# Kernel tuning notes

Measured on AMD Instinct MI355X. Metric: run time of the kernel, lower is better.

## Reference

```python
import jax, jax.numpy as jnp
import numpy as np

KERNEL = 3  # kernel_size from init_kwargs


def _unfold(x, k):
    """torch.nn.functional.unfold with padding=k//2, stride=1.
    Returns [b, c*k*k, h*w] with torch's ordering: index = c*(k*k) + kh*k + kw.
    """
    b, c, h, w = x.shape
    p = k // 2
    xp = jnp.pad(x, ((0, 0), (0, 0), (p, p), (p, p)))
    # fixed k*k = 9 slices (small static loop, not a data-dim loop)
    cols = jnp.stack(
        [xp[:, :, i:i + h, j:j + w] for i in range(k) for j in range(k)],
        axis=2,
    )  # [b, c, k*k, h, w]
    return cols.reshape(b, c * k * k, h * w)


def setup_inputs() -> dict:
    key = jax.random.key(0)
    k1, k2 = jax.random.split(key)
    x = jax.random.normal(k1, (8, 64, 128, 128), dtype=jnp.float32)
    # memory parameter: torch.rand -> uniform [0, 1), shape [c*k*k, out_channels]
    memory = jax.random.uniform(k2, (64 * KERNEL * KERNEL, 128), dtype=jnp.float32)
    return {"x": x, "memory": memory}


def reference(x, memory):
    b, c, h, w = x.shape
    cols = _unfold(x, KERNEL)                 # [b, c*k*k, h*w]
    cols = jax.nn.softmax(cols, axis=1)       # softmax over unfolded patch dim
    out = jnp.einsum('ki,bkl->bil', memory, cols)  # [b, out_ch, h*w]
    return out.reshape(b, memory.shape[1], h, w)
```

## Files before the change

kernel.cpp:

```cpp
#include <hip/hip_runtime.h>
#include <stdint.h>


#define Bn 8
#define Cn 64
#define Hn 128
#define Wn 128
#define OC 128
#define HW (Hn * Wn)

typedef __attribute__((ext_vector_type(8))) short bf16x8_t;
typedef __attribute__((ext_vector_type(4))) float f32x4_t;

__device__ inline unsigned short f2bf(float f) {
    union { float f; uint32_t u; } v; v.f = f;
    uint32_t u = v.u;
    u += 0x7fffu + ((u >> 16) & 1u);
    return (unsigned short)(u >> 16);
}
__device__ inline float bf2f(unsigned short h) {
    union { uint32_t u; float f; } v; v.u = ((uint32_t)h) << 16;
    return v.f;
}

__global__ void prep_b(const float* __restrict__ mem, unsigned short* __restrict__ Bt) {
    int kin = blockIdx.x;
    int n = threadIdx.x;
    int c = kin / 9, q = kin % 9;
    Bt[n * 576 + q * 64 + c] = f2bf(mem[kin * OC + n]);
}

__global__ __launch_bounds__(256) void exp_tr(const float* __restrict__ x,
                                              unsigned short* __restrict__ Et,
                                              float* __restrict__ S) {
    __shared__ __align__(16) unsigned short lds[128][72];
    int bid = blockIdx.x;
    int b = bid >> 7, h = bid & 127;
    int t = threadIdx.x;

    int c = t >> 2, l4 = t & 3;
    const float* xp = x + ((size_t)(b * Cn + c) * Hn + h) * Wn;
#pragma unroll
    for (int i = 0; i < 8; i++) {
        int w = i * 16 + l4 * 4;
        float4 v = *(const float4*)(xp + w);
        lds[w + 0][c] = f2bf(__expf(v.x));
        lds[w + 1][c] = f2bf(__expf(v.y));
        lds[w + 2][c] = f2bf(__expf(v.z));
        lds[w + 3][c] = f2bf(__expf(v.w));
    }
    __syncthreads();

    {
        int w = t >> 1, c0 = (t & 1) * 32;
        uint4* dst = (uint4*)(Et + (((size_t)(b * Hn + h) * Wn + w) * 64 + c0));
        const uint4* src = (const uint4*)(&lds[w][c0]);
        dst[0] = src[0]; dst[1] = src[1]; dst[2] = src[2]; dst[3] = src[3];
    }
    if (t < 128) {
        int w = t;
        float s = 0.f;
#pragma unroll
        for (int c2 = 0; c2 < 64; c2++) s += bf2f(lds[w][c2]);
        S[(size_t)(b * Hn + h) * Wn + w] = s;
    }
}

__global__ void boxz(const float* __restrict__ S, float* __restrict__ Zinv) {
    int p = blockIdx.x * 256 + threadIdx.x;
    int b = p >> 14, r = p & 16383, h = r >> 7, w = r & 127;
    const float* Sp = S + (size_t)b * HW;
    float z = 0.f;
#pragma unroll
    for (int dh = -1; dh <= 1; dh++) {
        int hh = h + dh;
#pragma unroll
        for (int dw = -1; dw <= 1; dw++) {
            int ww = w + dw;
            if (hh >= 0 && hh < Hn && ww >= 0 && ww < Wn)
                z += Sp[hh * Wn + ww];
            else
                z += 64.0f;
        }
    }
    Zinv[p] = 1.f / z;
}

__global__ __launch_bounds__(256) void conv_mfma(const unsigned short* __restrict__ Et,
                                                 const unsigned short* __restrict__ Bt,
                                                 const float* __restrict__ Zinv,
                                                 float* __restrict__ out) {
    __shared__ __align__(16) unsigned short lds[6 * 18 * 72];

    int bid = blockIdx.x;
    int b = bid >> 8;
    int rem = bid & 255;
    int ty = rem >> 3;
    int tx = rem & 7;
    int h0 = ty * 4, w0 = tx * 16;
    int t = threadIdx.x;

    {
        int pp = t >> 3;
        int c0 = (t & 7) * 8;
        const uint4 ones = make_uint4(0x3F803F80u, 0x3F803F80u, 0x3F803F80u, 0x3F803F80u);
#pragma unroll
        for (int rr = 0; rr < 4; rr++) {
            int p = pp + rr * 32;
            if (p < 108) {
                int y = p / 18, xx = p % 18;
                int gh = h0 - 1 + y, gw = w0 - 1 + xx;
                uint4 v = ones;
                if (gh >= 0 && gh < Hn && gw >= 0 && gw < Wn)
                    v = *(const uint4*)(Et + (((size_t)(b * Hn + gh) * Wn + gw) * 64 + c0));
                *(uint4*)(&lds[(y * 18 + xx) * 72 + c0]) = v;
            }
        }
    }
    __syncthreads();

    int wave = t >> 6, lane = t & 63;
    int mcol = lane & 15;
    int quad = lane >> 4;
    int koff = quad * 8;

    f32x4_t acc[4][2];
#pragma unroll
    for (int i = 0; i < 4; i++)
#pragma unroll
        for (int j = 0; j < 2; j++) acc[i][j] = (f32x4_t){0.f, 0.f, 0.f, 0.f};

    int n_base = wave * 32;

    for (int kc = 0; kc < 18; kc++) {
        int q = kc >> 1;
        int c0 = (kc & 1) * 32;
        int kh = q / 3, kw = q % 3;

        bf16x8_t a[4];
#pragma unroll
        for (int tI = 0; tI < 4; tI++) {
            int addr = ((tI + kh) * 18 + (mcol + kw)) * 72 + c0 + koff;
            a[tI] = *(const bf16x8_t*)(&lds[addr]);
        }
        bf16x8_t bb[2];
#pragma unroll
        for (int nn = 0; nn < 2; nn++) {
            int n = n_base + nn * 16 + mcol;
            bb[nn] = *(const bf16x8_t*)(Bt + (n * 576 + q * 64 + c0 + koff));
        }
#pragma unroll
        for (int tI = 0; tI < 4; tI++)
#pragma unroll
            for (int nn = 0; nn < 2; nn++)
                acc[tI][nn] = __builtin_amdgcn_mfma_f32_16x16x32_bf16(a[tI], bb[nn], acc[tI][nn], 0, 0, 0);
    }

    int xoff = quad * 4;
#pragma unroll
    for (int tI = 0; tI < 4; tI++) {
        int hy = h0 + tI;
        f32x4_t zi = *(const f32x4_t*)(Zinv + ((size_t)b * HW + hy * Wn + w0 + xoff));
#pragma unroll
        for (int nn = 0; nn < 2; nn++) {
            int n = n_base + nn * 16 + mcol;
            f32x4_t v = acc[tI][nn] * zi;
            *(f32x4_t*)(out + (((size_t)(b * OC + n) * Hn + hy) * Wn + w0 + xoff)) = v;
        }
    }
}

extern "C" void kernel_launch(void* const* d_in, const int* in_sizes, int n_in,
                              void* d_out, int out_size, void* d_ws, size_t ws_size,
                              hipStream_t stream) {
    const float* x = (const float*)d_in[0];
    const float* mem = (const float*)d_in[1];
    float* out = (float*)d_out;
    char* ws = (char*)d_ws;

    unsigned short* Et = (unsigned short*)(ws);
    unsigned short* Bt = (unsigned short*)(ws + 16777216);
    float* S   = (float*)(ws + 16924672);
    float* Zinv = (float*)(ws + 17448960);

    prep_b<<<576, 128, 0, stream>>>(mem, Bt);
    exp_tr<<<1024, 256, 0, stream>>>(x, Et, S);
    boxz<<<512, 256, 0, stream>>>(S, Zinv);
    conv_mfma<<<2048, 256, 0, stream>>>(Et, Bt, Zinv, out);
}
```

Before: 138.2 us.

## Fuse exp, normalizer box-sum and MFMA conv into one tiled kernel

Replaces the exp/transpose, box-sum and conv kernels with one kernel. Each block loads an 18x18 halo tile of x, computes exp into swizzled LDS along with per-pixel channel sums, builds the 3x3 normalizer in LDS, then runs 32x32x16 bf16 MFMAs with double-buffered fragment loads. This removes the global round-trips for the bf16 exp tensor, S and Zinv, plus two launches. In exchange, halo pixels are recomputed, x is read with scalar strided loads, and there are only 512 blocks with a large register footprint.

```diff
diff --git a/kernel.cpp b/kernel.cpp
--- a/kernel.cpp
+++ b/kernel.cpp
@@ -2,7 +2,6 @@
 #include <stdint.h>
 
 
-#define Bn 8
 #define Cn 64
 #define Hn 128
 #define Wn 128
@@ -11,6 +10,7 @@
 
 typedef __attribute__((ext_vector_type(8))) short bf16x8_t;
 typedef __attribute__((ext_vector_type(4))) float f32x4_t;
+typedef __attribute__((ext_vector_type(16))) float f32x16_t;
 
 __device__ inline unsigned short f2bf(float f) {
     union { float f; uint32_t u; } v; v.f = f;
@@ -30,142 +30,142 @@
     Bt[n * 576 + q * 64 + c] = f2bf(mem[kin * OC + n]);
 }
 
-__global__ __launch_bounds__(256) void exp_tr(const float* __restrict__ x,
-                                              unsigned short* __restrict__ Et,
-                                              float* __restrict__ S) {
-    __shared__ __align__(16) unsigned short lds[128][72];
+__global__ __launch_bounds__(256, 2) void fused_conv(const float* __restrict__ x,
+                                                     const unsigned short* __restrict__ Bt,
+                                                     float* __restrict__ out) {
+    __shared__ __align__(16) unsigned short Et[324 * 72];
+    __shared__ __align__(16) float St[324];
+    __shared__ __align__(16) float Zt[256];
+
     int bid = blockIdx.x;
-    int b = bid >> 7, h = bid & 127;
+    int b = bid >> 6;
+    int ty = (bid >> 3) & 7, tx = bid & 7;
+    int h0 = ty * 16, w0 = tx * 16;
     int t = threadIdx.x;
 
-    int c = t >> 2, l4 = t & 3;
-    const float* xp = x + ((size_t)(b * Cn + c) * Hn + h) * Wn;
+    const float* xb = x + (size_t)b * Cn * HW;
+
+    int y0 = t / 18, x0 = t - y0 * 18;
+    int p1 = t + 256;
+    int y1 = p1 / 18, x1 = p1 - y1 * 18;
+    bool v1 = (p1 < 324);
+    int gy0 = h0 - 1 + y0, gx0 = w0 - 1 + x0;
+    int gy1 = h0 - 1 + y1, gx1 = w0 - 1 + x1;
+    bool in0 = (gy0 >= 0 && gy0 < Hn && gx0 >= 0 && gx0 < Wn);
+    bool in1 = v1 && (gy1 >= 0 && gy1 < Hn && gx1 >= 0 && gx1 < Wn);
+    int idx0 = in0 ? (gy0 * Wn + gx0) : 0;
+    int idx1 = in1 ? (gy1 * Wn + gx1) : 0;
+    int sw0 = t & 3, sw1 = p1 & 3;
+
+    float s0 = 0.f, s1 = 0.f;
+#pragma unroll 4
+    for (int c = 0; c < 64; c++) {
+        int cpos_hi = (c >> 4), cpos_lo = (c & 15);
+        float va = xb[(size_t)c * HW + idx0];
+        va = in0 ? va : 0.f;
+        float ea = __expf(va);
+        unsigned short ha = f2bf(ea);
+        s0 += bf2f(ha);
+        Et[t * 72 + (((cpos_hi ^ sw0) << 4) | cpos_lo)] = ha;
+        if (v1) {
+            float vb = xb[(size_t)c * HW + idx1];
+            vb = in1 ? vb : 0.f;
+            float eb = __expf(vb);
+            unsigned short hb = f2bf(eb);
+            s1 += bf2f(hb);
+            Et[p1 * 72 + (((cpos_hi ^ sw1) << 4) | cpos_lo)] = hb;
+        }
+    }
+    St[t] = s0;
+    if (v1) St[p1] = s1;
+    __syncthreads();
+
+    {
+        int zy = t >> 4, zx = t & 15;
+        float z = 0.f;
 #pragma unroll
-    for (int i = 0; i < 8; i++) {
-        int w = i * 16 + l4 * 4;
-        float4 v = *(const float4*)(xp + w);
-        lds[w + 0][c] = f2bf(__expf(v.x));
-        lds[w + 1][c] = f2bf(__expf(v.y));
-        lds[w + 2][c] = f2bf(__expf(v.z));
-        lds[w + 3][c] = f2bf(__expf(v.w));
+        for (int dy = 0; dy < 3; dy++)
+#pragma unroll
+            for (int dx = 0; dx < 3; dx++)
+                z += St[(zy + dy) * 18 + (zx + dx)];
+        Zt[t] = 1.0f / z;
     }
     __syncthreads();
 
-    {
-        int w = t >> 1, c0 = (t & 1) * 32;
-        uint4* dst = (uint4*)(Et + (((size_t)(b * Hn + h) * Wn + w) * 64 + c0));
-        const uint4* src = (const uint4*)(&lds[w][c0]);
-        dst[0] = src[0]; dst[1] = src[1]; dst[2] = src[2]; dst[3] = src[3];
-    }
-    if (t < 128) {
-        int w = t;
-        float s = 0.f;
+    int lane = t & 63;
+    int wv = t >> 6;
+    int m = lane & 31;
+    int hi = lane >> 5;
+
+    int prb[2];
 #pragma unroll
-        for (int c2 = 0; c2 < 64; c2++) s += bf2f(lds[w][c2]);
-        S[(size_t)(b * Hn + h) * Wn + w] = s;
-    }
-}
+    for (int i = 0; i < 2; i++)
+        prb[i] = (wv * 4 + i * 2 + (m >> 4)) * 18 + (m & 15);
 
-__global__ void boxz(const float* __restrict__ S, float* __restrict__ Zinv) {
-    int p = blockIdx.x * 256 + threadIdx.x;
-    int b = p >> 14, r = p & 16383, h = r >> 7, w = r & 127;
-    const float* Sp = S + (size_t)b * HW;
-    float z = 0.f;
+    const unsigned short* bp[4];
 #pragma unroll
-    for (int dh = -1; dh <= 1; dh++) {
-        int hh = h + dh;
+    for (int nb = 0; nb < 4; nb++)
+        bp[nb] = Bt + (size_t)(nb * 32 + m) * 576 + hi * 8;
+
+    f32x16_t acc[2][4];
 #pragma unroll
-        for (int dw = -1; dw <= 1; dw++) {
-            int ww = w + dw;
-            if (hh >= 0 && hh < Hn && ww >= 0 && ww < Wn)
-                z += Sp[hh * Wn + ww];
-            else
-                z += 64.0f;
+    for (int i = 0; i < 2; i++)
+#pragma unroll
+        for (int nb = 0; nb < 4; nb++)
+#pragma unroll
+            for (int r = 0; r < 16; r++) acc[i][nb][r] = 0.f;
+
+    bf16x8_t Af[2][2], Bf[2][4];
+
+    auto loadK = [&](int kc, bf16x8_t* Ad, bf16x8_t* Bd) {
+        int q = kc >> 2;
+        int c0b = kc & 3;
+        int kh = q / 3, kw = q - kh * 3;
+        int poff = kh * 18 + kw;
+#pragma unroll
+        for (int i = 0; i < 2; i++) {
+            int pix = prb[i] + poff;
+            int a16 = pix * 72 + (((c0b ^ (pix & 3)) << 4) | (hi * 8));
+            Ad[i] = *(const bf16x8_t*)&Et[a16];
         }
-    }
-    Zinv[p] = 1.f / z;
-}
+        int boff = q * 64 + c0b * 16;
+#pragma unroll
+        for (int nb = 0; nb < 4; nb++)
+            Bd[nb] = *(const bf16x8_t*)(bp[nb] + boff);
+    };
 
-__global__ __launch_bounds__(256) void conv_mfma(const unsigned short* __restrict__ Et,
-                                                 const unsigned short* __restrict__ Bt,
-                                                 const float* __restrict__ Zinv,
-                                                 float* __restrict__ out) {
-    __shared__ __align__(16) unsigned short lds[6 * 18 * 72];
-
-    int bid = blockIdx.x;
-    int b = bid >> 8;
-    int rem = bid & 255;
-    int ty = rem >> 3;
-    int tx = rem & 7;
-    int h0 = ty * 4, w0 = tx * 16;
-    int t = threadIdx.x;
-
-    {
-        int pp = t >> 3;
-        int c0 = (t & 7) * 8;
-        const uint4 ones = make_uint4(0x3F803F80u, 0x3F803F80u, 0x3F803F80u, 0x3F803F80u);
+    loadK(0, Af[0], Bf[0]);
+#pragma unroll 2
+    for (int kc = 0; kc < 36; kc++) {
+        int cur = kc & 1, nxt = cur ^ 1;
+        if (kc + 1 < 36) loadK(kc + 1, Af[nxt], Bf[nxt]);
 #pragma unroll
-        for (int rr = 0; rr < 4; rr++) {
-            int p = pp + rr * 32;
-            if (p < 108) {
-                int y = p / 18, xx = p % 18;
-                int gh = h0 - 1 + y, gw = w0 - 1 + xx;
-                uint4 v = ones;
-                if (gh >= 0 && gh < Hn && gw >= 0 && gw < Wn)
-                    v = *(const uint4*)(Et + (((size_t)(b * Hn + gh) * Wn + gw) * 64 + c0));
-                *(uint4*)(&lds[(y * 18 + xx) * 72 + c0]) = v;
-            }
-        }
-    }
-    __syncthreads();
-
-    int wave = t >> 6, lane = t & 63;
-    int mcol = lane & 15;
-    int quad = lane >> 4;
-    int koff = quad * 8;
-
-    f32x4_t acc[4][2];
+        for (int i = 0; i < 2; i++)
 #pragma unroll
-    for (int i = 0; i < 4; i++)
-#pragma unroll
-        for (int j = 0; j < 2; j++) acc[i][j] = (f32x4_t){0.f, 0.f, 0.f, 0.f};
-
-    int n_base = wave * 32;
-
-    for (int kc = 0; kc < 18; kc++) {
-        int q = kc >> 1;
-        int c0 = (kc & 1) * 32;
-        int kh = q / 3, kw = q % 3;
-
-        bf16x8_t a[4];
-#pragma unroll
-        for (int tI = 0; tI < 4; tI++) {
-            int addr = ((tI + kh) * 18 + (mcol + kw)) * 72 + c0 + koff;
-            a[tI] = *(const bf16x8_t*)(&lds[addr]);
-        }
-        bf16x8_t bb[2];
-#pragma unroll
-        for (int nn = 0; nn < 2; nn++) {
-            int n = n_base + nn * 16 + mcol;
-            bb[nn] = *(const bf16x8_t*)(Bt + (n * 576 + q * 64 + c0 + koff));
-        }
-#pragma unroll
-        for (int tI = 0; tI < 4; tI++)
-#pragma unroll
-            for (int nn = 0; nn < 2; nn++)
-                acc[tI][nn] = __builtin_amdgcn_mfma_f32_16x16x32_bf16(a[tI], bb[nn], acc[tI][nn], 0, 0, 0);
+            for (int nb = 0; nb < 4; nb++)
+                acc[i][nb] = __builtin_amdgcn_mfma_f32_32x32x16_bf16(
+                    Af[cur][i], Bf[cur][nb], acc[i][nb], 0, 0, 0);
     }
 
-    int xoff = quad * 4;
 #pragma unroll
-    for (int tI = 0; tI < 4; tI++) {
-        int hy = h0 + tI;
-        f32x4_t zi = *(const f32x4_t*)(Zinv + ((size_t)b * HW + hy * Wn + w0 + xoff));
+    for (int i = 0; i < 2; i++) {
+        int mtg = wv * 2 + i;
 #pragma unroll
-        for (int nn = 0; nn < 2; nn++) {
-            int n = n_base + nn * 16 + mcol;
-            f32x4_t v = acc[tI][nn] * zi;
-            *(f32x4_t*)(out + (((size_t)(b * OC + n) * Hn + hy) * Wn + w0 + xoff)) = v;
+        for (int g = 0; g < 4; g++) {
+            int poff = g * 8 + hi * 4;
+            int p = mtg * 32 + poff;
+            int yy = p >> 4, xx = p & 15;
+            f32x4_t zi = *(const f32x4_t*)&Zt[p];
+            float* op = out + ((size_t)(b * OC + m) * HW + (h0 + yy) * Wn + (w0 + xx));
+#pragma unroll
+            for (int nb = 0; nb < 4; nb++) {
+                f32x4_t v;
+                v.x = acc[i][nb][g * 4 + 0] * zi.x;
+                v.y = acc[i][nb][g * 4 + 1] * zi.y;
+                v.z = acc[i][nb][g * 4 + 2] * zi.z;
+                v.w = acc[i][nb][g * 4 + 3] * zi.w;
+                *(f32x4_t*)(op + (size_t)nb * 32 * HW) = v;
+            }
         }
     }
 }
@@ -178,13 +178,8 @@
     float* out = (float*)d_out;
     char* ws = (char*)d_ws;
 
-    unsigned short* Et = (unsigned short*)(ws);
-    unsigned short* Bt = (unsigned short*)(ws + 16777216);
-    float* S   = (float*)(ws + 16924672);
-    float* Zinv = (float*)(ws + 17448960);
+    unsigned short* Bt = (unsigned short*)ws;
 
     prep_b<<<576, 128, 0, stream>>>(mem, Bt);
-    exp_tr<<<1024, 256, 0, stream>>>(x, Et, S);
-    boxz<<<512, 256, 0, stream>>>(S, Zinv);
-    conv_mfma<<<2048, 256, 0, stream>>>(Et, Bt, Zinv, out);
+    fused_conv<<<512, 256, 0, stream>>>(x, Bt, out);
 }
```

Measured after the change: 164.5 us. +19.0%, slower.
